# Kernel tuning notes

Measured on AMD Instinct MI355X. Metric: run time of the kernel, lower is better.

## Reference

```python
import jax, jax.numpy as jnp
import numpy as np

N_NODES = 100000


def _gcn_conv(x, W, b, src, dst, n):
    # PyG GCNConv: h = x @ W; add self-loops; norm = d^-1/2[src] * d^-1/2[dst];
    # out[i] = sum_{(s->i)} norm * h[s] + b
    h = x @ W  # [N, F_out]
    deg = jax.ops.segment_sum(jnp.ones_like(dst, dtype=h.dtype), dst, num_segments=n)
    dis = jnp.where(deg > 0, jax.lax.rsqrt(jnp.maximum(deg, 1.0)), 0.0)
    norm = dis[src] * dis[dst]  # [E]
    msg = h[src] * norm[:, None]  # [E, F_out] gather + scale
    out = jax.ops.segment_sum(msg, dst, num_segments=n)  # scatter-add
    return out + b


def _add_self_loops(edge_index, n):
    loops = jnp.arange(n, dtype=edge_index.dtype)
    src = jnp.concatenate([edge_index[0], loops])
    dst = jnp.concatenate([edge_index[1], loops])
    return src, dst


def setup_inputs() -> dict:
    key = jax.random.key(0)
    k_x, k_e, k_w1, k_w2 = jax.random.split(key, 4)
    n, e, f_in, f_hid = N_NODES, 1600000, 128, 64
    x = jax.random.normal(k_x, (n, f_in), dtype=jnp.float32)
    edge_index = jax.random.randint(k_e, (2, e), 0, n, dtype=jnp.int64)
    # Glorot-ish init for weights
    W1 = jax.random.normal(k_w1, (f_in, f_hid), dtype=jnp.float32) / np.sqrt(f_in)
    b1 = jnp.zeros((f_hid,), dtype=jnp.float32)
    W2 = jax.random.normal(k_w2, (f_hid, f_hid), dtype=jnp.float32) / np.sqrt(f_hid)
    b2 = jnp.zeros((f_hid,), dtype=jnp.float32)
    return {"x": x, "edge_index": edge_index, "W1": W1, "b1": b1, "W2": W2, "b2": b2}


def reference(x, edge_index, W1, b1, W2, b2):
    n = x.shape[0]
    src, dst = _add_self_loops(edge_index, n)
    h = jax.nn.relu(_gcn_conv(x, W1, b1, src, dst, n))
    # F.dropout(training=False) in eval mode is identity
    out = _gcn_conv(h, W2, b2, src, dst, n)
    return out
```

## Files before the change

kernel.cpp:

```cpp
#include <hip/hip_runtime.h>
#include <hip/hip_bf16.h>


#define FOUT 64
#define BW 128
#define BSH 7
#define MAXB 1024
#define CHUNK 4096
#define SLAB 3072

#define NT1 1024
#define NT2 512
#define LCOLN 2048

__device__ __forceinline__ float bf2f(unsigned int u16) {
    union { unsigned int i; float f; } c;
    c.i = u16 << 16;
    return c.f;
}
__device__ __forceinline__ unsigned short f2bf(float f) {
    union { float f; unsigned int i; } c;
    c.f = f;
    unsigned int i = c.i;
    return (unsigned short)((i + 0x7FFFu + ((i >> 16) & 1u)) >> 16);
}

typedef __attribute__((ext_vector_type(8))) short short8v;
typedef __attribute__((ext_vector_type(4))) float f32x4;

__device__ __forceinline__ void split_frag(const float* xa, short8v* Ah, short8v* Al) {
    union { unsigned int u[4]; short8v v; } H, L;
#pragma unroll
    for (int p = 0; p < 4; p++) {
        unsigned short h0 = f2bf(xa[2 * p]);
        unsigned short h1 = f2bf(xa[2 * p + 1]);
        H.u[p] = (unsigned int)h0 | ((unsigned int)h1 << 16);
        unsigned short l0 = f2bf(xa[2 * p] - bf2f(h0));
        unsigned short l1 = f2bf(xa[2 * p + 1] - bf2f(h1));
        L.u[p] = (unsigned int)l0 | ((unsigned int)l1 << 16);
    }
    *Ah = H.v;
    *Al = L.v;
}

__device__ __forceinline__ void conv_w_frag(const float* __restrict__ W,
                                            unsigned short* __restrict__ WhF,
                                            unsigned short* __restrict__ WlF,
                                            int task) {
    const int lane = task & 63;
    const int cf = (task >> 6) & 3;
    const int s = task >> 8;
    const int q = lane >> 4, m = lane & 15;
#pragma unroll
    for (int j = 0; j < 8; j++) {
        int k = s * 32 + q * 8 + j;
        float x = W[(size_t)k * 64 + cf * 16 + m];
        unsigned short h = f2bf(x);
        WhF[(size_t)task * 8 + j] = h;
        WlF[(size_t)task * 8 + j] = f2bf(x - bf2f(h));
    }
}

__global__ __launch_bounds__(512) void edge_hist(
    const int* __restrict__ dst, int* __restrict__ cnt, int E,
    const float* __restrict__ W1, const float* __restrict__ W2,
    unsigned short* __restrict__ whf1, unsigned short* __restrict__ wlf1,
    unsigned short* __restrict__ whf2, unsigned short* __restrict__ wlf2) {
    __shared__ int h[MAXB];
    const int blk = blockIdx.x, t = threadIdx.x;
    h[t] = 0;
    h[t + 512] = 0;
    __syncthreads();
    const int e0 = blk * CHUNK;
#pragma unroll
    for (int k = 0; k < CHUNK / 512; k++) {
        int e = e0 + k * 512 + t;
        if (e < E) atomicAdd(&h[dst[e] >> BSH], 1);
    }
    if (blk == 0) {
        for (int task = t; task < NT1 + NT2; task += 512) {
            if (task < NT1) conv_w_frag(W1, whf1, wlf1, task);
            else            conv_w_frag(W2, whf2, wlf2, task - NT1);
        }
    }
    __syncthreads();
    cnt[blk * MAXB + t] = h[t];
    cnt[blk * MAXB + t + 512] = h[t + 512];
}

__global__ __launch_bounds__(512) void col_scan(int* __restrict__ cnt, int nblk,
                                                int* __restrict__ gcnt) {
    __shared__ int ts[512];
    const int b = blockIdx.x;
    const int t = threadIdx.x;
    int v = (t < nblk) ? cnt[t * MAXB + b] : 0;
    ts[t] = v;
    __syncthreads();
    for (int off = 1; off < 512; off <<= 1) {
        int x = (t >= off) ? ts[t - off] : 0;
        __syncthreads();
        ts[t] += x;
        __syncthreads();
    }
    if (t < nblk) cnt[t * MAXB + b] = b * SLAB + ts[t] - v;
    if (t == 511) gcnt[b] = ts[511];
}

__global__ __launch_bounds__(512) void edge_place(
    const int* __restrict__ src, const int* __restrict__ dst,
    const int* __restrict__ cnt, int* __restrict__ ebuf, int E) {
    __shared__ int lbase[MAXB];
    __shared__ int cur[MAXB];
    const int blk = blockIdx.x, t = threadIdx.x;
    lbase[t] = cnt[blk * MAXB + t];
    lbase[t + 512] = cnt[blk * MAXB + t + 512];
    cur[t] = 0;
    cur[t + 512] = 0;
    __syncthreads();
    const int e0 = blk * CHUNK;
#pragma unroll
    for (int k = 0; k < CHUNK / 512; k++) {
        int e = e0 + k * 512 + t;
        if (e < E) {
            int d = dst[e];
            int b = d >> BSH;
            int r = atomicAdd(&cur[b], 1);
            ebuf[lbase[b] + r] = src[e] | ((d & (BW - 1)) << 17);
        }
    }
}

__global__ __launch_bounds__(256, 3) void csr_gemm(
    int* __restrict__ ebuf, const int* __restrict__ gcnt,
    unsigned int* __restrict__ rowinfo, float* __restrict__ dis, int n,
    const float* __restrict__ X, const unsigned short* __restrict__ WhF,
    const unsigned short* __restrict__ WlF, unsigned short* __restrict__ HS) {
    __shared__ int ldeg[BW];
    __shared__ float sdis[BW];
    __shared__ int wtot[2];
    const int b = blockIdx.x, t = threadIdx.x;
    const int node0 = b << BSH;
    const int nn = min(BW, n - node0);
    const int ebeg = b * SLAB;

    const int lane = t & 63;
    const int wvv = t >> 6;
    const int m = lane & 15;
    const int q = lane >> 4;
    const int tile0 = wvv * 2, tile1 = wvv * 2 + 1;
    const int r0 = node0 + tile0 * 16 + m;
    const int r1 = node0 + tile1 * 16 + m;
    const bool ok0 = (r0 < n), ok1 = (r1 < n);
    const float* xp0 = X + (size_t)r0 * 128 + q * 8;
    const float* xp1 = X + (size_t)r1 * 128 + q * 8;
    const float4 zf4 = make_float4(0.f, 0.f, 0.f, 0.f);

    float4 c00 = zf4, c01 = zf4, c10 = zf4, c11 = zf4;
    float4 d00 = zf4, d01 = zf4, d10 = zf4, d11 = zf4;
    if (ok0) {
        c00 = *(const float4*)xp0;        c01 = *(const float4*)(xp0 + 4);
        d00 = *(const float4*)(xp0 + 32); d01 = *(const float4*)(xp0 + 36);
    }
    if (ok1) {
        c10 = *(const float4*)xp1;        c11 = *(const float4*)(xp1 + 4);
        d10 = *(const float4*)(xp1 + 32); d11 = *(const float4*)(xp1 + 36);
    }

    int raw[SLAB / 256];
#pragma unroll
    for (int k = 0; k < SLAB / 256; k++) raw[k] = ebuf[ebeg + t + k * 256];

    const int cnt = gcnt[b];
    if (t < BW) ldeg[t] = 0;
    __syncthreads();

    int w[SLAB / 256];
#pragma unroll
    for (int k = 0; k < SLAB / 256; k++) {
        w[k] = (t + k * 256 < cnt) ? raw[k] : -1;
        if (w[k] >= 0) atomicAdd(&ldeg[w[k] >> 17], 1);
    }
    __syncthreads();

    int v = 0, pv = 0;
    if (t < BW) { v = ldeg[t]; pv = v; }
#pragma unroll
    for (int d = 1; d < 64; d <<= 1) {
        int x = __shfl_up(pv, d);
        if (lane >= d) pv += x;
    }
    if (t < BW && lane == 63) wtot[t >> 6] = pv;
    __syncthreads();
    if (t < BW && t >= 64) pv += wtot[0];
    const int ex = pv - v;
    if (t < nn) {
        rowinfo[node0 + t] = ((unsigned int)(ebeg + ex) << 8) | (unsigned int)v;
        float dv = rsqrtf((float)v + 1.0f);
        dis[node0 + t] = dv;
        sdis[t] = dv;
    } else if (t < BW) {
        sdis[t] = 0.f;
    }
    if (t < BW) ldeg[t] = ex;
    __syncthreads();
#pragma unroll
    for (int k = 0; k < SLAB / 256; k++)
        if (w[k] >= 0) {
            int r = atomicAdd(&ldeg[w[k] >> 17], 1);
            ebuf[ebeg + r] = w[k] & 0x1FFFF;
        }

    f32x4 acc0[4], acc1[4];
#pragma unroll
    for (int cf = 0; cf < 4; cf++) { acc0[cf] = (f32x4)0.f; acc1[cf] = (f32x4)0.f; }
    float4 n00, n01, n10, n11;

#define GSTEP(S)                                                                        \
    {                                                                                   \
        if ((S) + 2 < 4) {                                                              \
            n00 = zf4; n01 = zf4; n10 = zf4; n11 = zf4;                                 \
            if (ok0) { n00 = *(const float4*)(xp0 + ((S) + 2) * 32);                    \
                       n01 = *(const float4*)(xp0 + ((S) + 2) * 32 + 4); }              \
            if (ok1) { n10 = *(const float4*)(xp1 + ((S) + 2) * 32);                    \
                       n11 = *(const float4*)(xp1 + ((S) + 2) * 32 + 4); }              \
        }                                                                               \
        const unsigned short* wh = WhF + ((size_t)((S) * 4) * 64 + lane) * 8;           \
        const unsigned short* wl = WlF + ((size_t)((S) * 4) * 64 + lane) * 8;           \
        short8v Ah, Al;                                                                 \
        {                                                                               \
            const float xa[8] = {c00.x, c00.y, c00.z, c00.w, c01.x, c01.y, c01.z, c01.w}; \
            split_frag(xa, &Ah, &Al);                                                   \
        }                                                                               \
        _Pragma("unroll")                                                               \
        for (int cf = 0; cf < 4; cf++) {                                                \
            short8v bh = *(const short8v*)(wh + (size_t)cf * 64 * 8);                   \
            short8v bl = *(const short8v*)(wl + (size_t)cf * 64 * 8);                   \
            acc0[cf] = __builtin_amdgcn_mfma_f32_16x16x32_bf16(Ah, bh, acc0[cf], 0, 0, 0); \
            acc0[cf] = __builtin_amdgcn_mfma_f32_16x16x32_bf16(Al, bh, acc0[cf], 0, 0, 0); \
            acc0[cf] = __builtin_amdgcn_mfma_f32_16x16x32_bf16(Ah, bl, acc0[cf], 0, 0, 0); \
        }                                                                               \
        {                                                                               \
            const float xa[8] = {c10.x, c10.y, c10.z, c10.w, c11.x, c11.y, c11.z, c11.w}; \
            split_frag(xa, &Ah, &Al);                                                   \
        }                                                                               \
        _Pragma("unroll")                                                               \
        for (int cf = 0; cf < 4; cf++) {                                                \
            short8v bh = *(const short8v*)(wh + (size_t)cf * 64 * 8);                   \
            short8v bl = *(const short8v*)(wl + (size_t)cf * 64 * 8);                   \
            acc1[cf] = __builtin_amdgcn_mfma_f32_16x16x32_bf16(Ah, bh, acc1[cf], 0, 0, 0); \
            acc1[cf] = __builtin_amdgcn_mfma_f32_16x16x32_bf16(Al, bh, acc1[cf], 0, 0, 0); \
            acc1[cf] = __builtin_amdgcn_mfma_f32_16x16x32_bf16(Ah, bl, acc1[cf], 0, 0, 0); \
        }                                                                               \
        c00 = d00; c01 = d01; c10 = d10; c11 = d11;                                     \
        d00 = n00; d01 = n01; d10 = n10; d11 = n11;                                     \
    }
    GSTEP(0) GSTEP(1) GSTEP(2) GSTEP(3)
#undef GSTEP

#pragma unroll
    for (int r = 0; r < 4; r++) {
        int row = node0 + tile0 * 16 + q * 4 + r;
        if (row < n) {
            float dr = sdis[tile0 * 16 + q * 4 + r];
#pragma unroll
            for (int cf = 0; cf < 4; cf++)
                HS[(size_t)row * FOUT + cf * 16 + m] = f2bf(acc0[cf][r] * dr);
        }
        row = node0 + tile1 * 16 + q * 4 + r;
        if (row < n) {
            float dr = sdis[tile1 * 16 + q * 4 + r];
#pragma unroll
            for (int cf = 0; cf < 4; cf++)
                HS[(size_t)row * FOUT + cf * 16 + m] = f2bf(acc1[cf][r] * dr);
        }
    }
}

__device__ __forceinline__ void acc8(const uint4 u, float* a) {
    a[0] += bf2f(u.x & 0xFFFFu); a[1] += bf2f(u.x >> 16);
    a[2] += bf2f(u.y & 0xFFFFu); a[3] += bf2f(u.y >> 16);
    a[4] += bf2f(u.z & 0xFFFFu); a[5] += bf2f(u.z >> 16);
    a[6] += bf2f(u.w & 0xFFFFu); a[7] += bf2f(u.w >> 16);
}

__device__ __forceinline__ void gather_rows(
    const uint4* __restrict__ hsv, const int* __restrict__ lcol,
    const int* __restrict__ col, bool uselds, int off, int beg, int deg,
    int jj, float* a) {
    const int full = deg & ~3;
    if (full > 0) {
        int s0 = uselds ? lcol[off]     : col[beg];
        int s1 = uselds ? lcol[off + 1] : col[beg + 1];
        int s2 = uselds ? lcol[off + 2] : col[beg + 2];
        int s3 = uselds ? lcol[off + 3] : col[beg + 3];
        uint4 A0 = hsv[(size_t)s0 * 8 + jj];
        uint4 A1 = hsv[(size_t)s1 * 8 + jj];
        uint4 A2 = hsv[(size_t)s2 * 8 + jj];
        uint4 A3 = hsv[(size_t)s3 * 8 + jj];
        for (int p = 4; p < full; p += 4) {
            int t0 = uselds ? lcol[off + p]     : col[beg + p];
            int t1 = uselds ? lcol[off + p + 1] : col[beg + p + 1];
            int t2 = uselds ? lcol[off + p + 2] : col[beg + p + 2];
            int t3 = uselds ? lcol[off + p + 3] : col[beg + p + 3];
            uint4 B0 = hsv[(size_t)t0 * 8 + jj];
            uint4 B1 = hsv[(size_t)t1 * 8 + jj];
            uint4 B2 = hsv[(size_t)t2 * 8 + jj];
            uint4 B3 = hsv[(size_t)t3 * 8 + jj];
            acc8(A0, a); acc8(A1, a); acc8(A2, a); acc8(A3, a);
            A0 = B0; A1 = B1; A2 = B2; A3 = B3;
        }
        acc8(A0, a); acc8(A1, a); acc8(A2, a); acc8(A3, a);
    }
    for (int p = full; p < deg; p++) {
        int s = uselds ? lcol[off + p] : col[beg + p];
        acc8(hsv[(size_t)s * 8 + jj], a);
    }
}

__device__ __forceinline__ void stage_cols(
    const unsigned int* __restrict__ rowinfo, const int* __restrict__ col,
    int* lcol, int* sbs, int i0, int n, int tid) {
    if (tid == 0) {
        int last = min(i0 + 31, n - 1);
        unsigned int r0 = rowinfo[i0];
        unsigned int rl = rowinfo[last];
        int base = (int)(r0 >> 8);
        sbs[0] = base;
        sbs[1] = (int)(rl >> 8) + (int)(rl & 255u) - base;
    }
    __syncthreads();
    const int span = sbs[1];
    if (span <= LCOLN) {
        const int base = sbs[0];
        for (int k = tid; k < span; k += 256) lcol[k] = col[base + k];
    }
    __syncthreads();
}

#define OSTR 68
__global__ __launch_bounds__(256) void agg_gemm(
    const uint4* __restrict__ hsv, const unsigned int* __restrict__ rowinfo,
    const int* __restrict__ col, const float* __restrict__ dis,
    const float* __restrict__ bias,
    const unsigned short* __restrict__ WhF2, const unsigned short* __restrict__ WlF2,
    unsigned short* __restrict__ HS2, int n) {
    __shared__ float so[32 * OSTR];
    __shared__ int lcol[LCOLN];
    __shared__ int sbs[2];
    const int tid = threadIdx.x;
    const int wv = tid >> 6;
    const int lane = tid & 63;
    const int g = lane >> 3;
    const int jj = lane & 7;
    const int lrow = wv * 8 + g;
    const int i0 = blockIdx.x * 32;
    const int i = i0 + lrow;

    const unsigned int info = (i < n) ? rowinfo[i] : 0u;
    uint4 su = make_uint4(0u, 0u, 0u, 0u);
    if (i < n) su = hsv[(size_t)i * 8 + jj];

    stage_cols(rowinfo, col, lcol, sbs, i0, n, tid);
    const int base = sbs[0], span = sbs[1];
    const bool uselds = (span <= LCOLN);

    float o[8];
#pragma unroll
    for (int p = 0; p < 8; p++) o[p] = 0.f;

    if (i < n) {
        const int beg = (int)(info >> 8);
        const int deg = (int)(info & 255u);
        const int off = beg - base;

        float a[8];
        a[0] = bf2f(su.x & 0xFFFFu); a[1] = bf2f(su.x >> 16);
        a[2] = bf2f(su.y & 0xFFFFu); a[3] = bf2f(su.y >> 16);
        a[4] = bf2f(su.z & 0xFFFFu); a[5] = bf2f(su.z >> 16);
        a[6] = bf2f(su.w & 0xFFFFu); a[7] = bf2f(su.w >> 16);

        gather_rows(hsv, lcol, col, uselds, off, beg, deg, jj, a);

        float d = dis[i];
        const float4* b4 = (const float4*)bias;
        float4 bb0 = b4[jj * 2];
        float4 bb1 = b4[jj * 2 + 1];
        o[0] = fmaxf(d * a[0] + bb0.x, 0.f);
        o[1] = fmaxf(d * a[1] + bb0.y, 0.f);
        o[2] = fmaxf(d * a[2] + bb0.z, 0.f);
        o[3] = fmaxf(d * a[3] + bb0.w, 0.f);
        o[4] = fmaxf(d * a[4] + bb1.x, 0.f);
        o[5] = fmaxf(d * a[5] + bb1.y, 0.f);
        o[6] = fmaxf(d * a[6] + bb1.z, 0.f);
        o[7] = fmaxf(d * a[7] + bb1.w, 0.f);
    }
    {
        float* sp = &so[lrow * OSTR + jj * 8];
        *(float4*)sp = make_float4(o[0], o[1], o[2], o[3]);
        *(float4*)(sp + 4) = make_float4(o[4], o[5], o[6], o[7]);
    }
    __syncthreads();

    const int tile = wv >> 1;
    const int ch = wv & 1;
    const int m = lane & 15;
    const int q = lane >> 4;
    f32x4 acc[2];
    acc[0] = (f32x4)0.f;
    acc[1] = (f32x4)0.f;
#pragma unroll
    for (int s = 0; s < 2; s++) {
        const float* ap = &so[(tile * 16 + m) * OSTR + s * 32 + q * 8];
        float4 v0 = *(const float4*)ap;
        float4 v1 = *(const float4*)(ap + 4);
        const float xa[8] = {v0.x, v0.y, v0.z, v0.w, v1.x, v1.y, v1.z, v1.w};
        short8v Ah, Al;
        split_frag(xa, &Ah, &Al);
#pragma unroll
        for (int c = 0; c < 2; c++) {
            int cf = ch * 2 + c;
            const unsigned short* wh = WhF2 + ((size_t)(s * 4 + cf) * 64 + lane) * 8;
            const unsigned short* wl = WlF2 + ((size_t)(s * 4 + cf) * 64 + lane) * 8;
            short8v bh = *(const short8v*)wh;
            short8v bl = *(const short8v*)wl;
            acc[c] = __builtin_amdgcn_mfma_f32_16x16x32_bf16(Ah, bh, acc[c], 0, 0, 0);
            acc[c] = __builtin_amdgcn_mfma_f32_16x16x32_bf16(Al, bh, acc[c], 0, 0, 0);
            acc[c] = __builtin_amdgcn_mfma_f32_16x16x32_bf16(Ah, bl, acc[c], 0, 0, 0);
        }
    }
#pragma unroll
    for (int r = 0; r < 4; r++) {
        int lr = tile * 16 + q * 4 + r;
        int i2 = blockIdx.x * 32 + lr;
        if (i2 < n) {
            float dr = dis[i2];
#pragma unroll
            for (int c = 0; c < 2; c++) {
                HS2[(size_t)i2 * FOUT + (ch * 2 + c) * 16 + m] = f2bf(acc[c][r] * dr);
            }
        }
    }
}

template <bool RELU>
__global__ __launch_bounds__(256) void aggregate(
    const uint4* __restrict__ hsv, const unsigned int* __restrict__ rowinfo,
    const int* __restrict__ col, const float* __restrict__ dis,
    const float* __restrict__ bias, float* __restrict__ out, int n) {
    __shared__ int lcol[LCOLN];
    __shared__ int sbs[2];
    const int tid = threadIdx.x;
    const int wv = tid >> 6;
    const int lane = tid & 63;
    const int g = lane >> 3;
    const int jj = lane & 7;
    const int i0 = blockIdx.x * 32;
    const int i = i0 + wv * 8 + g;

    const unsigned int info = (i < n) ? rowinfo[i] : 0u;
    uint4 su = make_uint4(0u, 0u, 0u, 0u);
    if (i < n) su = hsv[(size_t)i * 8 + jj];

    stage_cols(rowinfo, col, lcol, sbs, i0, n, tid);
    const int base = sbs[0], span = sbs[1];
    const bool uselds = (span <= LCOLN);

    if (i >= n) return;

    const int beg = (int)(info >> 8);
    const int deg = (int)(info & 255u);
    const int off = beg - base;

    float a[8];
    a[0] = bf2f(su.x & 0xFFFFu); a[1] = bf2f(su.x >> 16);
    a[2] = bf2f(su.y & 0xFFFFu); a[3] = bf2f(su.y >> 16);
    a[4] = bf2f(su.z & 0xFFFFu); a[5] = bf2f(su.z >> 16);
    a[6] = bf2f(su.w & 0xFFFFu); a[7] = bf2f(su.w >> 16);

    gather_rows(hsv, lcol, col, uselds, off, beg, deg, jj, a);

    float d = dis[i];
    const float4* b4 = (const float4*)bias;
    float4 bb0 = b4[jj * 2];
    float4 bb1 = b4[jj * 2 + 1];
    float4 o0, o1;
    o0.x = d * a[0] + bb0.x; o0.y = d * a[1] + bb0.y;
    o0.z = d * a[2] + bb0.z; o0.w = d * a[3] + bb0.w;
    o1.x = d * a[4] + bb1.x; o1.y = d * a[5] + bb1.y;
    o1.z = d * a[6] + bb1.z; o1.w = d * a[7] + bb1.w;
    if (RELU) {
        o0.x = fmaxf(o0.x, 0.f); o0.y = fmaxf(o0.y, 0.f);
        o0.z = fmaxf(o0.z, 0.f); o0.w = fmaxf(o0.w, 0.f);
        o1.x = fmaxf(o1.x, 0.f); o1.y = fmaxf(o1.y, 0.f);
        o1.z = fmaxf(o1.z, 0.f); o1.w = fmaxf(o1.w, 0.f);
    }
    float4* orow = (float4*)out + (size_t)i * 16 + jj * 2;
    orow[0] = o0;
    orow[1] = o1;
}

extern "C" void kernel_launch(void* const* d_in, const int* in_sizes, int n_in,
                              void* d_out, int out_size, void* d_ws, size_t ws_size,
                              hipStream_t stream) {
    const float* x  = (const float*)d_in[0];
    const int*   ei = (const int*)d_in[1];
    const float* W1 = (const float*)d_in[2];
    const float* b1 = (const float*)d_in[3];
    const float* W2 = (const float*)d_in[4];
    const float* b2 = (const float*)d_in[5];

    const int n = in_sizes[0] / 128;
    const int E = in_sizes[1] / 2;
    const int* srcp = ei;
    const int* dstp = ei + E;

    float* out = (float*)d_out;

    const int B = (n + BW - 1) / BW;
    const int nblk = (E + CHUNK - 1) / CHUNK;

    int*            cnt     = (int*)d_ws;
    int*            gcnt    = cnt + 512 * MAXB;
    unsigned int*   rowinfo = (unsigned int*)(gcnt + MAXB);
    float*          dis     = (float*)(rowinfo + n);
    int*            ebuf    = (int*)(dis + n);
    unsigned short* hs      = (unsigned short*)(ebuf + (size_t)B * SLAB);
    unsigned short* whf1    = hs + (size_t)n * FOUT;
    unsigned short* wlf1    = whf1 + (size_t)NT1 * 8;
    unsigned short* whf2    = wlf1 + (size_t)NT1 * 8;
    unsigned short* wlf2    = whf2 + (size_t)NT2 * 8;
    unsigned short* hs2     = wlf2 + (size_t)NT2 * 8;

    edge_hist<<<nblk, 512, 0, stream>>>(dstp, cnt, E, W1, W2,
                                        whf1, wlf1, whf2, wlf2);
    col_scan<<<B, 512, 0, stream>>>(cnt, nblk, gcnt);
    edge_place<<<nblk, 512, 0, stream>>>(srcp, dstp, cnt, ebuf, E);

    csr_gemm<<<B, 256, 0, stream>>>(ebuf, gcnt, rowinfo, dis, n,
                                    x, whf1, wlf1, hs);

    agg_gemm<<<(n + 31) / 32, 256, 0, stream>>>(
        (const uint4*)hs, rowinfo, ebuf, dis, b1, whf2, wlf2, hs2, n);

    aggregate<false><<<(n + 31) / 32, 256, 0, stream>>>(
        (const uint4*)hs2, rowinfo, ebuf, dis, b2, out, n);
}
```

Measured before the change: 212.1 us.

## Fuse edge histogram, scan and placement into one local-sort pass

Replaces the three-kernel global bucket sort (histogram, column scan, placement) with one kernel that sorts each 4096-edge chunk by destination bucket in shared memory and writes per-chunk packed offset/count tables. The GEMM kernel then rebuilds each bucket's edge list itself, doing a prefix scan over the chunk counts and a binary search to gather its edges from every chunk. This removes two kernel launches and the global scatter pass, at the cost of more scattered gathers and per-element binary search in csr_gemm. Packing offsets and counts into 16 bits, and capping the chunk count at 512, limit the supported input sizes.

```diff
diff --git a/kernel.cpp b/kernel.cpp
--- a/kernel.cpp
+++ b/kernel.cpp
@@ -6,6 +6,7 @@
 #define BW 128
 #define BSH 7
 #define MAXB 1024
+#define NCHS 512
 #define CHUNK 4096
 #define SLAB 3072
 
@@ -61,22 +62,34 @@
     }
 }
 
-__global__ __launch_bounds__(512) void edge_hist(
-    const int* __restrict__ dst, int* __restrict__ cnt, int E,
+__global__ __launch_bounds__(512) void edge_sort(
+    const int* __restrict__ src, const int* __restrict__ dst, int E,
+    int* __restrict__ pk, int* __restrict__ ebuf2,
     const float* __restrict__ W1, const float* __restrict__ W2,
     unsigned short* __restrict__ whf1, unsigned short* __restrict__ wlf1,
     unsigned short* __restrict__ whf2, unsigned short* __restrict__ wlf2) {
     __shared__ int h[MAXB];
+    __shared__ int lbuf[CHUNK];
+    __shared__ int wt8[8];
     const int blk = blockIdx.x, t = threadIdx.x;
+    const int lane = t & 63, wv = t >> 6;
+    const int e0 = blk * CHUNK;
+    const int chunkE = min(CHUNK, E - e0);
+
+    int ed[CHUNK / 512], es[CHUNK / 512];
+#pragma unroll
+    for (int k = 0; k < CHUNK / 512; k++) {
+        int e = e0 + k * 512 + t;
+        bool ok = (e < E);
+        ed[k] = ok ? dst[e] : -1;
+        es[k] = ok ? src[e] : 0;
+    }
     h[t] = 0;
     h[t + 512] = 0;
     __syncthreads();
-    const int e0 = blk * CHUNK;
-#pragma unroll
-    for (int k = 0; k < CHUNK / 512; k++) {
-        int e = e0 + k * 512 + t;
-        if (e < E) atomicAdd(&h[dst[e] >> BSH], 1);
-    }
+#pragma unroll
+    for (int k = 0; k < CHUNK / 512; k++)
+        if (ed[k] >= 0) atomicAdd(&h[ed[k] >> BSH], 1);
     if (blk == 0) {
         for (int task = t; task < NT1 + NT2; task += 512) {
             if (task < NT1) conv_w_frag(W1, whf1, wlf1, task);
@@ -84,60 +97,71 @@
         }
     }
     __syncthreads();
-    cnt[blk * MAXB + t] = h[t];
-    cnt[blk * MAXB + t + 512] = h[t + 512];
-}
-
-__global__ __launch_bounds__(512) void col_scan(int* __restrict__ cnt, int nblk,
-                                                int* __restrict__ gcnt) {
-    __shared__ int ts[512];
-    const int b = blockIdx.x;
-    const int t = threadIdx.x;
-    int v = (t < nblk) ? cnt[t * MAXB + b] : 0;
-    ts[t] = v;
-    __syncthreads();
-    for (int off = 1; off < 512; off <<= 1) {
-        int x = (t >= off) ? ts[t - off] : 0;
-        __syncthreads();
-        ts[t] += x;
-        __syncthreads();
-    }
-    if (t < nblk) cnt[t * MAXB + b] = b * SLAB + ts[t] - v;
-    if (t == 511) gcnt[b] = ts[511];
-}
-
-__global__ __launch_bounds__(512) void edge_place(
-    const int* __restrict__ src, const int* __restrict__ dst,
-    const int* __restrict__ cnt, int* __restrict__ ebuf, int E) {
-    __shared__ int lbase[MAXB];
-    __shared__ int cur[MAXB];
-    const int blk = blockIdx.x, t = threadIdx.x;
-    lbase[t] = cnt[blk * MAXB + t];
-    lbase[t + 512] = cnt[blk * MAXB + t + 512];
-    cur[t] = 0;
-    cur[t + 512] = 0;
-    __syncthreads();
-    const int e0 = blk * CHUNK;
+    const int c0 = h[t], c1 = h[t + 512];
+
+    int pv = c0;
+#pragma unroll
+    for (int d = 1; d < 64; d <<= 1) {
+        int x = __shfl_up(pv, d);
+        if (lane >= d) pv += x;
+    }
+    if (lane == 63) wt8[wv] = pv;
+    __syncthreads();
+    int woff = 0, tot0 = 0;
+#pragma unroll
+    for (int ww = 0; ww < 8; ww++) {
+        int vw = wt8[ww];
+        if (ww < wv) woff += vw;
+        tot0 += vw;
+    }
+    const int excl0 = woff + pv - c0;
+    __syncthreads();
+    int pv1 = c1;
+#pragma unroll
+    for (int d = 1; d < 64; d <<= 1) {
+        int x = __shfl_up(pv1, d);
+        if (lane >= d) pv1 += x;
+    }
+    if (lane == 63) wt8[wv] = pv1;
+    __syncthreads();
+    int woff1 = 0;
+#pragma unroll
+    for (int ww = 0; ww < 8; ww++)
+        if (ww < wv) woff1 += wt8[ww];
+    const int excl1 = tot0 + woff1 + pv1 - c1;
+
+    pk[t * NCHS + blk] = (excl0 << 16) | c0;
+    pk[(t + 512) * NCHS + blk] = (excl1 << 16) | c1;
+
+    h[t] = excl0;
+    h[t + 512] = excl1;
+    __syncthreads();
+#pragma unroll
+    for (int k = 0; k < CHUNK / 512; k++)
+        if (ed[k] >= 0) {
+            int b = ed[k] >> BSH;
+            int r = atomicAdd(&h[b], 1);
+            lbuf[r] = es[k] | ((ed[k] & (BW - 1)) << 17);
+        }
+    __syncthreads();
 #pragma unroll
     for (int k = 0; k < CHUNK / 512; k++) {
-        int e = e0 + k * 512 + t;
-        if (e < E) {
-            int d = dst[e];
-            int b = d >> BSH;
-            int r = atomicAdd(&cur[b], 1);
-            ebuf[lbase[b] + r] = src[e] | ((d & (BW - 1)) << 17);
-        }
+        int i = t + k * 512;
+        if (i < chunkE) ebuf2[(size_t)blk * CHUNK + i] = lbuf[i];
     }
 }
 
 __global__ __launch_bounds__(256, 3) void csr_gemm(
-    int* __restrict__ ebuf, const int* __restrict__ gcnt,
-    unsigned int* __restrict__ rowinfo, float* __restrict__ dis, int n,
+    const int* __restrict__ pk, const int* __restrict__ ebuf2, int nch,
+    int* __restrict__ ebuf, unsigned int* __restrict__ rowinfo,
+    float* __restrict__ dis, int n,
     const float* __restrict__ X, const unsigned short* __restrict__ WhF,
     const unsigned short* __restrict__ WlF, unsigned short* __restrict__ HS) {
     __shared__ int ldeg[BW];
     __shared__ float sdis[BW];
-    __shared__ int wtot[2];
+    __shared__ int wt4[4];
+    __shared__ int prefL[NCHS];
+    __shared__ int loffL[NCHS];
     const int b = blockIdx.x, t = threadIdx.x;
     const int node0 = b << BSH;
     const int nn = min(BW, n - node0);
@@ -155,6 +179,8 @@
     const float* xp1 = X + (size_t)r1 * 128 + q * 8;
     const float4 zf4 = make_float4(0.f, 0.f, 0.f, 0.f);
 
+    const int pkA = (t < nch) ? pk[b * NCHS + t] : 0;
+    const int pkB = (t + 256 < nch) ? pk[b * NCHS + t + 256] : 0;
     float4 c00 = zf4, c01 = zf4, c10 = zf4, c11 = zf4;
     float4 d00 = zf4, d01 = zf4, d10 = zf4, d11 = zf4;
     if (ok0) {
@@ -166,33 +192,80 @@
         d10 = *(const float4*)(xp1 + 32); d11 = *(const float4*)(xp1 + 36);
     }
 
-    int raw[SLAB / 256];
-#pragma unroll
-    for (int k = 0; k < SLAB / 256; k++) raw[k] = ebuf[ebeg + t + k * 256];
-
-    const int cnt = gcnt[b];
-    if (t < BW) ldeg[t] = 0;
-    __syncthreads();
-
-    int w[SLAB / 256];
-#pragma unroll
-    for (int k = 0; k < SLAB / 256; k++) {
-        w[k] = (t + k * 256 < cnt) ? raw[k] : -1;
-        if (w[k] >= 0) atomicAdd(&ldeg[w[k] >> 17], 1);
-    }
-    __syncthreads();
-
-    int v = 0, pv = 0;
-    if (t < BW) { v = ldeg[t]; pv = v; }
+    const int cA = pkA & 0xFFFF, cB = pkB & 0xFFFF;
+    int pv = cA;
 #pragma unroll
     for (int d = 1; d < 64; d <<= 1) {
         int x = __shfl_up(pv, d);
         if (lane >= d) pv += x;
     }
-    if (t < BW && lane == 63) wtot[t >> 6] = pv;
-    __syncthreads();
-    if (t < BW && t >= 64) pv += wtot[0];
-    const int ex = pv - v;
+    if (lane == 63) wt4[wvv] = pv;
+    __syncthreads();
+    int woff = 0, tot0 = 0;
+#pragma unroll
+    for (int ww = 0; ww < 4; ww++) {
+        int vw = wt4[ww];
+        if (ww < wvv) woff += vw;
+        tot0 += vw;
+    }
+    const int exA = woff + pv - cA;
+    __syncthreads();
+    int pv1 = cB;
+#pragma unroll
+    for (int d = 1; d < 64; d <<= 1) {
+        int x = __shfl_up(pv1, d);
+        if (lane >= d) pv1 += x;
+    }
+    if (lane == 63) wt4[wvv] = pv1;
+    __syncthreads();
+    int woff1 = 0, tot1 = 0;
+#pragma unroll
+    for (int ww = 0; ww < 4; ww++) {
+        int vw = wt4[ww];
+        if (ww < wvv) woff1 += vw;
+        tot1 += vw;
+    }
+    const int exB = tot0 + woff1 + pv1 - cB;
+    const int cntE = tot0 + tot1;
+    prefL[t] = exA;
+    prefL[t + 256] = exB;
+    loffL[t] = (int)((unsigned)pkA >> 16);
+    loffL[t + 256] = (int)((unsigned)pkB >> 16);
+    if (t < BW) ldeg[t] = 0;
+    __syncthreads();
+
+    int w[SLAB / 256];
+#pragma unroll
+    for (int k = 0; k < SLAB / 256; k++) {
+        const int p = t + k * 256;
+        if (p < cntE) {
+            int lo = 0, hi = NCHS;
+#pragma unroll
+            for (int it = 0; it < 9; it++) {
+                int mid = (lo + hi) >> 1;
+                if (prefL[mid] <= p) lo = mid; else hi = mid;
+            }
+            w[k] = ebuf2[(size_t)lo * CHUNK + loffL[lo] + (p - prefL[lo])];
+        } else {
+            w[k] = -1;
+        }
+    }
+#pragma unroll
+    for (int k = 0; k < SLAB / 256; k++)
+        if (w[k] >= 0) atomicAdd(&ldeg[w[k] >> 17], 1);
+    __syncthreads();
+
+    int v = 0, pv2 = 0;
+    if (t < BW) { v = ldeg[t]; pv2 = v; }
+#pragma unroll
+    for (int d = 1; d < 64; d <<= 1) {
+        int x = __shfl_up(pv2, d);
+        if (lane >= d) pv2 += x;
+    }
+    if (t < BW && lane == 63) wt4[t >> 6] = pv2;
+    __syncthreads();
+    if (t < BW && t >= 64) pv2 += wt4[0];
+    const int ex = pv2 - v;
     if (t < nn) {
         rowinfo[node0 + t] = ((unsigned int)(ebeg + ex) << 8) | (unsigned int)v;
         float dv = rsqrtf((float)v + 1.0f);
@@ -517,11 +590,11 @@
     float* out = (float*)d_out;
 
     const int B = (n + BW - 1) / BW;
-    const int nblk = (E + CHUNK - 1) / CHUNK;
-
-    int*            cnt     = (int*)d_ws;
-    int*            gcnt    = cnt + 512 * MAXB;
-    unsigned int*   rowinfo = (unsigned int*)(gcnt + MAXB);
+    const int nch = (E + CHUNK - 1) / CHUNK;
+
+    int*            pk      = (int*)d_ws;
+    int*            ebuf2   = pk + (size_t)MAXB * NCHS;
+    unsigned int*   rowinfo = (unsigned int*)(ebuf2 + (size_t)NCHS * CHUNK);
     float*          dis     = (float*)(rowinfo + n);
     int*            ebuf    = (int*)(dis + n);
     unsigned short* hs      = (unsigned short*)(ebuf + (size_t)B * SLAB);
@@ -531,12 +604,10 @@
     unsigned short* wlf2    = whf2 + (size_t)NT2 * 8;
     unsigned short* hs2     = wlf2 + (size_t)NT2 * 8;
 
-    edge_hist<<<nblk, 512, 0, stream>>>(dstp, cnt, E, W1, W2,
-                                        whf1, wlf1, whf2, wlf2);
-    col_scan<<<B, 512, 0, stream>>>(cnt, nblk, gcnt);
-    edge_place<<<nblk, 512, 0, stream>>>(srcp, dstp, cnt, ebuf, E);
-
-    csr_gemm<<<B, 256, 0, stream>>>(ebuf, gcnt, rowinfo, dis, n,
+    edge_sort<<<nch, 512, 0, stream>>>(srcp, dstp, E, pk, ebuf2, W1, W2,
+                                       whf1, wlf1, whf2, wlf2);
+
+    csr_gemm<<<B, 256, 0, stream>>>(pk, ebuf2, nch, ebuf, rowinfo, dis, n,
                                     x, whf1, wlf1, hs);
 
     agg_gemm<<<(n + 31) / 32, 256, 0, stream>>>(
```

Measured after the change: 203.9 us. 1.04x faster.
